# Kernel tuning notes

Hardware: AMD Instinct MI355X
Metric: run time of the kernel (lower is better)

## Reference

```python
import jax, jax.numpy as jnp
import numpy as np

N_HEAD = 16
ROPE_THETA = 10000.0


def _rope_cache(T, dim, theta=ROPE_THETA):
    # inv_freq over even indices, as in RotaryEmbedding
    inv_freq = 1.0 / (theta ** (jnp.arange(0, dim, 2, dtype=jnp.float32) / dim))
    freqs = jnp.arange(T, dtype=jnp.float32)[:, None] * inv_freq[None, :]  # [T, dim//2]
    return jnp.cos(freqs), jnp.sin(freqs)


def _apply_rope(x, cos, sin):
    # x: [B, H, T, D]; cos/sin: [T, D//2] broadcast over B,H
    x1 = x[..., ::2]
    x2 = x[..., 1::2]
    # even slots: x1*cos - x2*sin ; odd slots: x2*cos + x1*sin (interleaved rotate-pairs)
    r1 = x1 * cos - x2 * sin
    r2 = x2 * cos + x1 * sin
    return jnp.stack([r1, r2], axis=-1).reshape(x.shape)


def setup_inputs() -> dict:
    key = jax.random.key(0)
    k1, k2, k3 = jax.random.split(key, 3)
    B, T, C = 4, 2048, 1024
    x = jax.random.normal(k1, (B, T, C), dtype=jnp.float32)
    W_qkv = jax.random.normal(k2, (C, 3 * C), dtype=jnp.float32) * (C ** -0.5)
    W_out = jax.random.normal(k3, (C, C), dtype=jnp.float32) * (C ** -0.5)
    return {"x": x, "W_qkv": W_qkv, "W_out": W_out}


def reference(x, W_qkv, W_out):
    B, T, C = x.shape
    H = N_HEAD
    D = C // H
    # fused QKV projection -> [3, B, H, T, D]
    qkv = (x @ W_qkv).reshape(B, T, 3, H, D).transpose(2, 0, 3, 1, 4)
    q, k, v = qkv[0], qkv[1], qkv[2]
    cos, sin = _rope_cache(T, D)
    q = _apply_rope(q, cos, sin)
    k = _apply_rope(k, cos, sin)
    scale = 1.0 / jnp.sqrt(jnp.float32(D))
    scores = jnp.einsum('bhqd,bhkd->bhqk', q, k) * scale  # [B,H,T,T]
    causal_mask = jnp.tril(jnp.ones((T, T), dtype=bool))
    scores = jnp.where(causal_mask, scores, -jnp.inf)
    attn = jax.nn.softmax(scores, axis=-1)
    out = jnp.einsum('bhqk,bhkd->bhqd', attn, v)  # [B,H,T,D]
    out = out.transpose(0, 2, 1, 3).reshape(B, T, C)
    return out @ W_out
```

## Files before the change

### kernel.cpp

```cpp
#include <hip/hip_runtime.h>
#include <math.h>

#define BATCH 4
#define SEQ   2048
#define CDIM  1024
#define NHEAD 16
#define HDIM  64
#define QKVN  3072
#define QSCALE 0.1803368801111244f

typedef float f32x4 __attribute__((ext_vector_type(4)));
typedef short bf16x8 __attribute__((ext_vector_type(8)));
typedef short bf16x4 __attribute__((ext_vector_type(4)));

static __device__ __forceinline__ unsigned short f2bf(float f) {
    unsigned int u = __float_as_uint(f);
    u += 0x7FFF + ((u >> 16) & 1);
    return (unsigned short)(u >> 16);
}
static __device__ __forceinline__ float bf2f(unsigned short u) {
    return __uint_as_float(((unsigned int)u) << 16);
}
static __device__ __forceinline__ bf16x8 lds_read8(const unsigned short* p) {
    bf16x4 lo = *(const bf16x4*)p;
    bf16x4 hi = *(const bf16x4*)(p + 4);
    return __builtin_shufflevector(lo, hi, 0, 1, 2, 3, 4, 5, 6, 7);
}

__global__ __launch_bounds__(256) void convert_bf16(const float* __restrict__ src,
                                                    unsigned short* __restrict__ dst,
                                                    int n4) {
    int i = blockIdx.x * 256 + threadIdx.x;
    if (i >= n4) return;
    float4 v = ((const float4*)src)[i];
    ushort4 o;
    o.x = f2bf(v.x); o.y = f2bf(v.y); o.z = f2bf(v.z); o.w = f2bf(v.w);
    ((ushort4*)dst)[i] = o;
}

__global__ __launch_bounds__(256) void transpose_bf16(const float* __restrict__ W,
                                                      unsigned short* __restrict__ Wt,
                                                      int K, int N) {
    __shared__ unsigned short tile[64][65];
    const int tid = threadIdx.x;
    const int n0 = blockIdx.x * 64;
    const int k0 = blockIdx.y * 64;
    const int r = tid >> 4;
    const int c4 = (tid & 15) << 2;
    #pragma unroll
    for (int ii = 0; ii < 4; ii++) {
        int row = r + 16 * ii;
        float4 v = *(const float4*)&W[(size_t)(k0 + row) * N + n0 + c4];
        tile[c4 + 0][row] = f2bf(v.x);
        tile[c4 + 1][row] = f2bf(v.y);
        tile[c4 + 2][row] = f2bf(v.z);
        tile[c4 + 3][row] = f2bf(v.w);
    }
    __syncthreads();
    #pragma unroll
    for (int ii = 0; ii < 4; ii++) {
        int row = r + 16 * ii;
        ushort4 o;
        o.x = tile[row][c4 + 0];
        o.y = tile[row][c4 + 1];
        o.z = tile[row][c4 + 2];
        o.w = tile[row][c4 + 3];
        *(ushort4*)&Wt[(size_t)(n0 + row) * K + k0 + c4] = o;
    }
}

#define GLDS(gp, lp) __builtin_amdgcn_global_load_lds(                       \
    (const __attribute__((address_space(1))) unsigned int*)(gp),             \
    (__attribute__((address_space(3))) unsigned int*)(lp), 16, 0, 0)

template <typename OUT>
__global__ __launch_bounds__(256) void gemm_bt_bf16(
    const unsigned short* __restrict__ A,
    const unsigned short* __restrict__ Bt,
    OUT* __restrict__ C, int M, int N, int K) {
    __shared__ unsigned short As[128 * 32];
    __shared__ unsigned short Bs[128 * 32];

    const int tid = threadIdx.x;
    const int wave = tid >> 6;
    const int lane = tid & 63;
    const int bm = blockIdx.y * 128;
    const int bn = blockIdx.x * 128;
    const int wm = (wave >> 1) * 64;
    const int wn = (wave & 1) * 64;

    const int srow = tid >> 2;
    const int scol = (tid & 3) << 3;
    const unsigned short* Ag0 = A + (size_t)(bm + srow) * K + scol;
    const unsigned short* Ag1 = A + (size_t)(bm + 64 + srow) * K + scol;
    const unsigned short* Bg0 = Bt + (size_t)(bn + srow) * K + scol;
    const unsigned short* Bg1 = Bt + (size_t)(bn + 64 + srow) * K + scol;
    char* AsW = (char*)As + wave * 1024;
    char* BsW = (char*)Bs + wave * 1024;

    const int fm = lane & 15;
    const int fq = (lane >> 4) << 3;

    f32x4 acc[4][4];
    #pragma unroll
    for (int i = 0; i < 4; i++)
        #pragma unroll
        for (int j = 0; j < 4; j++)
            acc[i][j] = (f32x4){0.f, 0.f, 0.f, 0.f};

    for (int k0 = 0; k0 < K; k0 += 32) {
        GLDS(Ag0 + k0, AsW);
        GLDS(Ag1 + k0, AsW + 4096);
        GLDS(Bg0 + k0, BsW);
        GLDS(Bg1 + k0, BsW + 4096);
        __syncthreads();

        bf16x8 af[4], bfr[4];
        #pragma unroll
        for (int i = 0; i < 4; i++)
            af[i] = *(const bf16x8*)&As[(wm + i * 16 + fm) * 32 + fq];
        #pragma unroll
        for (int j = 0; j < 4; j++)
            bfr[j] = *(const bf16x8*)&Bs[(wn + j * 16 + fm) * 32 + fq];
        #pragma unroll
        for (int i = 0; i < 4; i++)
            #pragma unroll
            for (int j = 0; j < 4; j++)
                acc[i][j] = __builtin_amdgcn_mfma_f32_16x16x32_bf16(
                    af[i], bfr[j], acc[i][j], 0, 0, 0);
        __syncthreads();
    }

    const int er = (lane >> 4) * 4;
    #pragma unroll
    for (int i = 0; i < 4; i++) {
        #pragma unroll
        for (int j = 0; j < 4; j++) {
            #pragma unroll
            for (int r = 0; r < 4; r++) {
                size_t off = (size_t)(bm + wm + i * 16 + er + r) * N + bn + wn + j * 16 + fm;
                if constexpr (sizeof(OUT) == 2)
                    C[off] = f2bf(acc[i][j][r]);
                else
                    C[off] = acc[i][j][r];
            }
        }
    }
}

__global__ __launch_bounds__(256) void rope_qk(const unsigned short* __restrict__ qkvb,
                                               unsigned short* __restrict__ Qg,
                                               unsigned short* __restrict__ Kg) {
    const int i = blockIdx.x * 256 + threadIdx.x;
    const int c4 = (i & 15) << 2;
    const int h = (i >> 4) & 15;
    const int s = (i >> 8) & 1;
    const int t = (i >> 9) & 2047;
    const int b = i >> 20;

    ushort4 v = *(const ushort4*)&qkvb[(((size_t)(b * SEQ + t) * 3 + s) * CDIM) + h * HDIM + c4];
    float x0 = bf2f(v.x), x1 = bf2f(v.y), x2 = bf2f(v.z), x3 = bf2f(v.w);
    const float invf0 = powf(10000.0f, -((float)c4) / 64.0f);
    const float invf1 = powf(10000.0f, -((float)(c4 + 2)) / 64.0f);
    float s0, c0, s1, c1;
    __sincosf((float)t * invf0, &s0, &c0);
    __sincosf((float)t * invf1, &s1, &c1);
    const float sc = s == 0 ? QSCALE : 1.0f;
    ushort4 o;
    o.x = f2bf((x0 * c0 - x1 * s0) * sc);
    o.y = f2bf((x1 * c0 + x0 * s0) * sc);
    o.z = f2bf((x2 * c1 - x3 * s1) * sc);
    o.w = f2bf((x3 * c1 + x2 * s1) * sc);
    unsigned short* dst = (s == 0) ? Qg : Kg;
    *(ushort4*)&dst[((size_t)(b * NHEAD + h) * SEQ + t) * HDIM + c4] = o;
}

__global__ __launch_bounds__(256) void transpose_v(const unsigned short* __restrict__ qkvb,
                                                   unsigned short* __restrict__ Vtg) {
    __shared__ unsigned short tile[64 * 68];
    const int tid = threadIdx.x;
    const int tt = blockIdx.x;
    const int bh = blockIdx.y;
    const int b = bh >> 4, h = bh & 15;
    const int r = tid >> 4;
    const int c4 = (tid & 15) << 2;
    #pragma unroll
    for (int ii = 0; ii < 4; ii++) {
        int row = r + 16 * ii;
        ushort4 v = *(const ushort4*)&qkvb[(((size_t)(b * SEQ + tt * 64 + row) * 3 + 2) * CDIM) + h * HDIM + c4];
        *(ushort4*)&tile[row * 68 + c4] = v;
    }
    __syncthreads();
    #pragma unroll
    for (int ii = 0; ii < 4; ii++) {
        int d = r + 16 * ii;
        ushort4 o;
        o.x = tile[(c4 + 0) * 68 + d];
        o.y = tile[(c4 + 1) * 68 + d];
        o.z = tile[(c4 + 2) * 68 + d];
        o.w = tile[(c4 + 3) * 68 + d];
        *(ushort4*)&Vtg[((size_t)bh * HDIM + d) * SEQ + tt * 64 + c4] = o;
    }
}

__global__ __launch_bounds__(256, 3) void flash_attn_mfma(
    const unsigned short* __restrict__ Qg,
    const unsigned short* __restrict__ Kg,
    const unsigned short* __restrict__ Vtg,
    unsigned short* __restrict__ att) {
    __shared__ unsigned short Ks[64 * 68];
    __shared__ unsigned short Vt[64 * 68];
    __shared__ unsigned short Ps[128 * 68];

    const int tid = threadIdx.x;
    const int wave = tid >> 6;
    const int lane = tid & 63;
    const int fm = lane & 15;
    const int quad = lane >> 4;
    const int fq = quad << 3;
    const int wq = wave * 32;
    const int bh = blockIdx.x & 63;
    const int qt = 15 - (blockIdx.x >> 6);
    const int b = bh >> 4, h = bh & 15;

    const int r_ld = tid >> 4;
    const int c4 = (tid & 15) << 2;

    bf16x8 aq[2][2];
    #pragma unroll
    for (int i = 0; i < 2; i++)
        #pragma unroll
        for (int ks = 0; ks < 2; ks++)
            aq[i][ks] = *(const bf16x8*)&Qg[((size_t)bh * SEQ + qt * 128 + wq + i * 16 + fm) * HDIM + ks * 32 + fq];

    bf16x8 bones;
    #pragma unroll
    for (int z = 0; z < 8; z++) bones[z] = (short)0x3F80;

    f32x4 O[2][4], lsum[2];
    #pragma unroll
    for (int i = 0; i < 2; i++) {
        lsum[i] = (f32x4){0.f, 0.f, 0.f, 0.f};
        #pragma unroll
        for (int dt = 0; dt < 4; dt++) O[i][dt] = (f32x4){0.f, 0.f, 0.f, 0.f};
    }

    const int jtop = 2 * qt + 1;
    for (int j = 0; j <= jtop; j++) {
        #pragma unroll
        for (int ii = 0; ii < 4; ii++) {
            const int row = r_ld + 16 * ii;
            *(ushort4*)&Ks[row * 68 + c4] =
                *(const ushort4*)&Kg[((size_t)bh * SEQ + j * 64 + row) * HDIM + c4];
            *(ushort4*)&Vt[row * 68 + c4] =
                *(const ushort4*)&Vtg[((size_t)bh * HDIM + row) * SEQ + j * 64 + c4];
        }
        __syncthreads();

        const bool active = (j * 64) <= (qt * 128 + wq + 31);
        if (active) {
            f32x4 sa[2][4];
            #pragma unroll
            for (int i = 0; i < 2; i++)
                #pragma unroll
                for (int jj = 0; jj < 4; jj++)
                    sa[i][jj] = (f32x4){0.f, 0.f, 0.f, 0.f};
            #pragma unroll
            for (int ks = 0; ks < 2; ks++) {
                #pragma unroll
                for (int jj = 0; jj < 4; jj++) {
                    bf16x8 bk = lds_read8(&Ks[(jj * 16 + fm) * 68 + ks * 32 + fq]);
                    sa[0][jj] = __builtin_amdgcn_mfma_f32_16x16x32_bf16(aq[0][ks], bk, sa[0][jj], 0, 0, 0);
                    sa[1][jj] = __builtin_amdgcn_mfma_f32_16x16x32_bf16(aq[1][ks], bk, sa[1][jj], 0, 0, 0);
                }
            }

            if (j * 64 + 63 > qt * 128 + wq) {
                const int kb = j * 64 + fm;
                #pragma unroll
                for (int i = 0; i < 2; i++) {
                    const int rb = qt * 128 + wq + i * 16 + quad * 4;
                    #pragma unroll
                    for (int jj = 0; jj < 4; jj++)
                        #pragma unroll
                        for (int r = 0; r < 4; r++)
                            if (kb + jj * 16 > rb + r) sa[i][jj][r] = -INFINITY;
                }
            }

            #pragma unroll
            for (int i = 0; i < 2; i++) {
                const int prow = (wq + i * 16 + quad * 4) * 68 + fm;
                #pragma unroll
                for (int jj = 0; jj < 4; jj++)
                    #pragma unroll
                    for (int r = 0; r < 4; r++)
                        Ps[prow + r * 68 + jj * 16] = f2bf(exp2f(sa[i][jj][r]));
            }

            #pragma unroll
            for (int ks = 0; ks < 2; ks++) {
                bf16x8 ap0 = lds_read8(&Ps[(wq + fm) * 68 + ks * 32 + fq]);
                bf16x8 ap1 = lds_read8(&Ps[(wq + 16 + fm) * 68 + ks * 32 + fq]);
                lsum[0] = __builtin_amdgcn_mfma_f32_16x16x32_bf16(ap0, bones, lsum[0], 0, 0, 0);
                lsum[1] = __builtin_amdgcn_mfma_f32_16x16x32_bf16(ap1, bones, lsum[1], 0, 0, 0);
                #pragma unroll
                for (int dt = 0; dt < 4; dt++) {
                    bf16x8 bv = lds_read8(&Vt[(dt * 16 + fm) * 68 + ks * 32 + fq]);
                    O[0][dt] = __builtin_amdgcn_mfma_f32_16x16x32_bf16(ap0, bv, O[0][dt], 0, 0, 0);
                    O[1][dt] = __builtin_amdgcn_mfma_f32_16x16x32_bf16(ap1, bv, O[1][dt], 0, 0, 0);
                }
            }
        }
        __syncthreads();
    }

    #pragma unroll
    for (int i = 0; i < 2; i++) {
        #pragma unroll
        for (int r = 0; r < 4; r++) {
            const float inv_l = 1.0f / lsum[i][r];
            const int row = qt * 128 + wq + i * 16 + quad * 4 + r;
            #pragma unroll
            for (int dt = 0; dt < 4; dt++)
                att[(size_t)(b * SEQ + row) * CDIM + h * HDIM + dt * 16 + fm] =
                    f2bf(O[i][dt][r] * inv_l);
        }
    }
}

extern "C" void kernel_launch(void* const* d_in, const int* in_sizes, int n_in,
                              void* d_out, int out_size, void* d_ws, size_t ws_size,
                              hipStream_t stream) {
    const float* x     = (const float*)d_in[0];
    const float* W_qkv = (const float*)d_in[1];
    const float* W_out = (const float*)d_in[2];
    float* out = (float*)d_out;

    const int M = BATCH * SEQ;

    unsigned short* qkvb = (unsigned short*)d_ws;
    unsigned short* xb   = qkvb + (size_t)M * QKVN;
    unsigned short* wqb  = xb + (size_t)M * CDIM;
    unsigned short* wob  = wqb + (size_t)CDIM * QKVN;
    unsigned short* attb = wob + (size_t)CDIM * CDIM;
    unsigned short* Qg   = attb + (size_t)M * CDIM;
    unsigned short* Kg   = Qg + (size_t)M * CDIM;
    unsigned short* Vtg  = Kg + (size_t)M * CDIM;

    convert_bf16<<<(M * CDIM / 4 + 255) / 256, 256, 0, stream>>>(x, xb, M * CDIM / 4);
    transpose_bf16<<<dim3(QKVN / 64, CDIM / 64), 256, 0, stream>>>(W_qkv, wqb, CDIM, QKVN);
    transpose_bf16<<<dim3(CDIM / 64, CDIM / 64), 256, 0, stream>>>(W_out, wob, CDIM, CDIM);

    gemm_bt_bf16<unsigned short><<<dim3(QKVN / 128, M / 128), 256, 0, stream>>>(
        xb, wqb, qkvb, M, QKVN, CDIM);

    rope_qk<<<(BATCH * SEQ * 2 * NHEAD * 16) / 256, 256, 0, stream>>>(qkvb, Qg, Kg);
    transpose_v<<<dim3(SEQ / 64, BATCH * NHEAD), 256, 0, stream>>>(qkvb, Vtg);

    flash_attn_mfma<<<BATCH * NHEAD * (SEQ / 128), 256, 0, stream>>>(Qg, Kg, Vtg, attb);

    gemm_bt_bf16<float><<<dim3(CDIM / 128, M / 128), 256, 0, stream>>>(
        attb, wob, out, M, CDIM, CDIM);
}
```

Measured before the change: 311.6 us.

## Fuse x conversion and RoPE into QKV GEMM, swizzle LDS layout

Removes the separate fp32-to-bf16 conversion of x by loading fp32 x directly in the QKV GEMM, converting it in registers and storing it to LDS. The GEMM epilogue applies RoPE and the Q scale using a lane shuffle to fetch each pair partner, and writes Q, K and V straight into head-major layout, which removes the rope_qk kernel and the qkvb intermediate. Both GEMMs also gain an XOR swizzle on LDS columns to reduce bank conflicts. The trade-off is that the A operand now uses synchronous register loads instead of async global-to-LDS copies, and the epilogue does scattered 2-byte stores with sincos work per element.

```diff
diff --git a/kernel.cpp b/kernel.cpp
--- a/kernel.cpp
+++ b/kernel.cpp
@@ -1,4 +1,5 @@
 #include <hip/hip_runtime.h>
+#include <hip/hip_bf16.h>
 #include <math.h>
 
 #define BATCH 4
@@ -8,6 +9,7 @@
 #define HDIM  64
 #define QKVN  3072
 #define QSCALE 0.1803368801111244f
+#define LOG2_10K_64 0.2076205059f
 
 typedef float f32x4 __attribute__((ext_vector_type(4)));
 typedef short bf16x8 __attribute__((ext_vector_type(8)));
@@ -18,24 +20,14 @@
     u += 0x7FFF + ((u >> 16) & 1);
     return (unsigned short)(u >> 16);
 }
-static __device__ __forceinline__ float bf2f(unsigned short u) {
-    return __uint_as_float(((unsigned int)u) << 16);
+static __device__ __forceinline__ unsigned int pk2bf(float lo, float hi) {
+    __hip_bfloat162 h = __float22bfloat162_rn(make_float2(lo, hi));
+    return *(unsigned int*)&h;
 }
 static __device__ __forceinline__ bf16x8 lds_read8(const unsigned short* p) {
     bf16x4 lo = *(const bf16x4*)p;
     bf16x4 hi = *(const bf16x4*)(p + 4);
     return __builtin_shufflevector(lo, hi, 0, 1, 2, 3, 4, 5, 6, 7);
-}
-
-__global__ __launch_bounds__(256) void convert_bf16(const float* __restrict__ src,
-                                                    unsigned short* __restrict__ dst,
-                                                    int n4) {
-    int i = blockIdx.x * 256 + threadIdx.x;
-    if (i >= n4) return;
-    float4 v = ((const float4*)src)[i];
-    ushort4 o;
-    o.x = f2bf(v.x); o.y = f2bf(v.y); o.z = f2bf(v.z); o.w = f2bf(v.w);
-    ((ushort4*)dst)[i] = o;
 }
 
 __global__ __launch_bounds__(256) void transpose_bf16(const float* __restrict__ W,
@@ -73,11 +65,14 @@
     (const __attribute__((address_space(1))) unsigned int*)(gp),             \
     (__attribute__((address_space(3))) unsigned int*)(lp), 16, 0, 0)
 
-template <typename OUT>
-__global__ __launch_bounds__(256) void gemm_bt_bf16(
-    const unsigned short* __restrict__ A,
+
+__global__ __launch_bounds__(256) void gemm_qkv(
+    const float* __restrict__ Af,
     const unsigned short* __restrict__ Bt,
-    OUT* __restrict__ C, int M, int N, int K) {
+    unsigned short* __restrict__ Qg,
+    unsigned short* __restrict__ Kg,
+    unsigned short* __restrict__ Vg) {
+    const int K = CDIM, N = QKVN;
     __shared__ unsigned short As[128 * 32];
     __shared__ unsigned short Bs[128 * 32];
 
@@ -90,7 +85,108 @@
     const int wn = (wave & 1) * 64;
 
     const int srow = tid >> 2;
-    const int scol = (tid & 3) << 3;
+    const int slot = tid & 3;
+    const int scol = ((slot ^ ((tid >> 3) & 3)) << 3);
+    const float* Af0 = Af + (size_t)(bm + srow) * K + scol;
+    const float* Af1 = Af + (size_t)(bm + 64 + srow) * K + scol;
+    const unsigned short* Bg0 = Bt + (size_t)(bn + srow) * K + scol;
+    const unsigned short* Bg1 = Bt + (size_t)(bn + 64 + srow) * K + scol;
+    unsigned int* AsD0 = (unsigned int*)&As[srow * 32 + slot * 8];
+    unsigned int* AsD1 = (unsigned int*)&As[(64 + srow) * 32 + slot * 8];
+    char* BsW = (char*)Bs + wave * 1024;
+
+    const int fm = lane & 15;
+    const int quad = lane >> 4;
+    const int ck = (quad ^ ((fm >> 1) & 3)) << 3;
+
+    f32x4 acc[4][4];
+    #pragma unroll
+    for (int i = 0; i < 4; i++)
+        #pragma unroll
+        for (int j = 0; j < 4; j++)
+            acc[i][j] = (f32x4){0.f, 0.f, 0.f, 0.f};
+
+    for (int k0 = 0; k0 < K; k0 += 32) {
+        float4 a0 = *(const float4*)(Af0 + k0);
+        float4 a1 = *(const float4*)(Af0 + k0 + 4);
+        float4 a2 = *(const float4*)(Af1 + k0);
+        float4 a3 = *(const float4*)(Af1 + k0 + 4);
+        GLDS(Bg0 + k0, BsW);
+        GLDS(Bg1 + k0, BsW + 4096);
+        uint4 w0 = {pk2bf(a0.x, a0.y), pk2bf(a0.z, a0.w), pk2bf(a1.x, a1.y), pk2bf(a1.z, a1.w)};
+        uint4 w1 = {pk2bf(a2.x, a2.y), pk2bf(a2.z, a2.w), pk2bf(a3.x, a3.y), pk2bf(a3.z, a3.w)};
+        *(uint4*)AsD0 = w0;
+        *(uint4*)AsD1 = w1;
+        __syncthreads();
+
+        bf16x8 af[4], bfr[4];
+        #pragma unroll
+        for (int i = 0; i < 4; i++)
+            af[i] = *(const bf16x8*)&As[(wm + i * 16 + fm) * 32 + ck];
+        #pragma unroll
+        for (int j = 0; j < 4; j++)
+            bfr[j] = *(const bf16x8*)&Bs[(wn + j * 16 + fm) * 32 + ck];
+        #pragma unroll
+        for (int i = 0; i < 4; i++)
+            #pragma unroll
+            for (int j = 0; j < 4; j++)
+                acc[i][j] = __builtin_amdgcn_mfma_f32_16x16x32_bf16(
+                    af[i], bfr[j], acc[i][j], 0, 0, 0);
+        __syncthreads();
+    }
+
+    const int s = bn >> 10;
+    unsigned short* dst = (s == 0) ? Qg : (s == 1) ? Kg : Vg;
+    const float osc = (s == 0) ? QSCALE : 1.0f;
+    const int er = quad * 4;
+    #pragma unroll
+    for (int j = 0; j < 4; j++) {
+        const int n = bn + wn + j * 16 + fm;
+        const int h = (n >> 6) & 15;
+        const int d = n & 63;
+        const float invf = exp2f(-(float)(d & ~1) * LOG2_10K_64);
+        const float sgn = (d & 1) ? 1.0f : -1.0f;
+        #pragma unroll
+        for (int i = 0; i < 4; i++) {
+            #pragma unroll
+            for (int r = 0; r < 4; r++) {
+                const int row = bm + wm + i * 16 + er + r;
+                const int b = row >> 11;
+                const int t = row & 2047;
+                float v = acc[i][j][r];
+                float res;
+                if (s < 2) {
+                    const float partner = __shfl_xor(v, 1, 64);
+                    float sn, cs;
+                    __sincosf((float)t * invf, &sn, &cs);
+                    res = (v * cs + sgn * partner * sn) * osc;
+                } else {
+                    res = v;
+                }
+                dst[(((size_t)(b * NHEAD + h) * SEQ) + t) * HDIM + d] = f2bf(res);
+            }
+        }
+    }
+}
+
+__global__ __launch_bounds__(256) void gemm_out(
+    const unsigned short* __restrict__ A,
+    const unsigned short* __restrict__ Bt,
+    float* __restrict__ C) {
+    const int K = CDIM, N = CDIM;
+    __shared__ unsigned short As[128 * 32];
+    __shared__ unsigned short Bs[128 * 32];
+
+    const int tid = threadIdx.x;
+    const int wave = tid >> 6;
+    const int lane = tid & 63;
+    const int bm = blockIdx.y * 128;
+    const int bn = blockIdx.x * 128;
+    const int wm = (wave >> 1) * 64;
+    const int wn = (wave & 1) * 64;
+
+    const int srow = tid >> 2;
+    const int scol = (((tid & 3) ^ ((tid >> 3) & 3)) << 3);
     const unsigned short* Ag0 = A + (size_t)(bm + srow) * K + scol;
     const unsigned short* Ag1 = A + (size_t)(bm + 64 + srow) * K + scol;
     const unsigned short* Bg0 = Bt + (size_t)(bn + srow) * K + scol;
@@ -99,7 +195,8 @@
     char* BsW = (char*)Bs + wave * 1024;
 
     const int fm = lane & 15;
-    const int fq = (lane >> 4) << 3;
+    const int quad = lane >> 4;
+    const int ck = (quad ^ ((fm >> 1) & 3)) << 3;
 
     f32x4 acc[4][4];
     #pragma unroll
@@ -118,10 +215,10 @@
         bf16x8 af[4], bfr[4];
         #pragma unroll
         for (int i = 0; i < 4; i++)
-            af[i] = *(const bf16x8*)&As[(wm + i * 16 + fm) * 32 + fq];
+            af[i] = *(const bf16x8*)&As[(wm + i * 16 + fm) * 32 + ck];
         #pragma unroll
         for (int j = 0; j < 4; j++)
-            bfr[j] = *(const bf16x8*)&Bs[(wn + j * 16 + fm) * 32 + fq];
+            bfr[j] = *(const bf16x8*)&Bs[(wn + j * 16 + fm) * 32 + ck];
         #pragma unroll
         for (int i = 0; i < 4; i++)
             #pragma unroll
@@ -131,63 +228,29 @@
         __syncthreads();
     }
 
-    const int er = (lane >> 4) * 4;
-    #pragma unroll
-    for (int i = 0; i < 4; i++) {
-        #pragma unroll
-        for (int j = 0; j < 4; j++) {
-            #pragma unroll
-            for (int r = 0; r < 4; r++) {
-                size_t off = (size_t)(bm + wm + i * 16 + er + r) * N + bn + wn + j * 16 + fm;
-                if constexpr (sizeof(OUT) == 2)
-                    C[off] = f2bf(acc[i][j][r]);
-                else
-                    C[off] = acc[i][j][r];
-            }
-        }
-    }
-}
-
-__global__ __launch_bounds__(256) void rope_qk(const unsigned short* __restrict__ qkvb,
-                                               unsigned short* __restrict__ Qg,
-                                               unsigned short* __restrict__ Kg) {
-    const int i = blockIdx.x * 256 + threadIdx.x;
-    const int c4 = (i & 15) << 2;
-    const int h = (i >> 4) & 15;
-    const int s = (i >> 8) & 1;
-    const int t = (i >> 9) & 2047;
-    const int b = i >> 20;
-
-    ushort4 v = *(const ushort4*)&qkvb[(((size_t)(b * SEQ + t) * 3 + s) * CDIM) + h * HDIM + c4];
-    float x0 = bf2f(v.x), x1 = bf2f(v.y), x2 = bf2f(v.z), x3 = bf2f(v.w);
-    const float invf0 = powf(10000.0f, -((float)c4) / 64.0f);
-    const float invf1 = powf(10000.0f, -((float)(c4 + 2)) / 64.0f);
-    float s0, c0, s1, c1;
-    __sincosf((float)t * invf0, &s0, &c0);
-    __sincosf((float)t * invf1, &s1, &c1);
-    const float sc = s == 0 ? QSCALE : 1.0f;
-    ushort4 o;
-    o.x = f2bf((x0 * c0 - x1 * s0) * sc);
-    o.y = f2bf((x1 * c0 + x0 * s0) * sc);
-    o.z = f2bf((x2 * c1 - x3 * s1) * sc);
-    o.w = f2bf((x3 * c1 + x2 * s1) * sc);
-    unsigned short* dst = (s == 0) ? Qg : Kg;
-    *(ushort4*)&dst[((size_t)(b * NHEAD + h) * SEQ + t) * HDIM + c4] = o;
-}
-
-__global__ __launch_bounds__(256) void transpose_v(const unsigned short* __restrict__ qkvb,
+    const int er = quad * 4;
+    #pragma unroll
+    for (int i = 0; i < 4; i++)
+        #pragma unroll
+        for (int j = 0; j < 4; j++)
+            #pragma unroll
+            for (int r = 0; r < 4; r++)
+                C[(size_t)(bm + wm + i * 16 + er + r) * N + bn + wn + j * 16 + fm] =
+                    acc[i][j][r];
+}
+
+__global__ __launch_bounds__(256) void transpose_v(const unsigned short* __restrict__ Vg,
                                                    unsigned short* __restrict__ Vtg) {
     __shared__ unsigned short tile[64 * 68];
     const int tid = threadIdx.x;
     const int tt = blockIdx.x;
     const int bh = blockIdx.y;
-    const int b = bh >> 4, h = bh & 15;
     const int r = tid >> 4;
     const int c4 = (tid & 15) << 2;
     #pragma unroll
     for (int ii = 0; ii < 4; ii++) {
         int row = r + 16 * ii;
-        ushort4 v = *(const ushort4*)&qkvb[(((size_t)(b * SEQ + tt * 64 + row) * 3 + 2) * CDIM) + h * HDIM + c4];
+        ushort4 v = *(const ushort4*)&Vg[((size_t)bh * SEQ + tt * 64 + row) * HDIM + c4];
         *(ushort4*)&tile[row * 68 + c4] = v;
     }
     __syncthreads();
@@ -339,27 +402,22 @@
 
     const int M = BATCH * SEQ;
 
-    unsigned short* qkvb = (unsigned short*)d_ws;
-    unsigned short* xb   = qkvb + (size_t)M * QKVN;
-    unsigned short* wqb  = xb + (size_t)M * CDIM;
+    unsigned short* wqb  = (unsigned short*)d_ws;
     unsigned short* wob  = wqb + (size_t)CDIM * QKVN;
     unsigned short* attb = wob + (size_t)CDIM * CDIM;
     unsigned short* Qg   = attb + (size_t)M * CDIM;
     unsigned short* Kg   = Qg + (size_t)M * CDIM;
-    unsigned short* Vtg  = Kg + (size_t)M * CDIM;
-
-    convert_bf16<<<(M * CDIM / 4 + 255) / 256, 256, 0, stream>>>(x, xb, M * CDIM / 4);
+    unsigned short* Vg   = Kg + (size_t)M * CDIM;
+    unsigned short* Vtg  = Vg + (size_t)M * CDIM;
+
     transpose_bf16<<<dim3(QKVN / 64, CDIM / 64), 256, 0, stream>>>(W_qkv, wqb, CDIM, QKVN);
     transpose_bf16<<<dim3(CDIM / 64, CDIM / 64), 256, 0, stream>>>(W_out, wob, CDIM, CDIM);
 
-    gemm_bt_bf16<unsigned short><<<dim3(QKVN / 128, M / 128), 256, 0, stream>>>(
-        xb, wqb, qkvb, M, QKVN, CDIM);
-
-    rope_qk<<<(BATCH * SEQ * 2 * NHEAD * 16) / 256, 256, 0, stream>>>(qkvb, Qg, Kg);
-    transpose_v<<<dim3(SEQ / 64, BATCH * NHEAD), 256, 0, stream>>>(qkvb, Vtg);
+    gemm_qkv<<<dim3(QKVN / 128, M / 128), 256, 0, stream>>>(x, wqb, Qg, Kg, Vg);
+
+    transpose_v<<<dim3(SEQ / 64, BATCH * NHEAD), 256, 0, stream>>>(Vg, Vtg);
 
     flash_attn_mfma<<<BATCH * NHEAD * (SEQ / 128), 256, 0, stream>>>(Qg, Kg, Vtg, attb);
 
-    gemm_bt_bf16<float><<<dim3(CDIM / 128, M / 128), 256, 0, stream>>>(
-        attb, wob, out, M, CDIM, CDIM);
-}
+    gemm_out<<<dim3(CDIM / 128, M / 128), 256, 0, stream>>>(attb, wob, out);
+}
```

Result: slower. 327.1 us (+5.0%).
